# Optimization experiments

Measured on AMD Instinct MI355X. Metric: run time of the kernel, lower is better.

The kernel has to match this reference:

```python
import jax, jax.numpy as jnp
import numpy as np

DIM = 512          # model dim
DH = 32            # dim_head
WSZ = 8            # window_size
HEADS = DIM // DH  # 16
INNER = HEADS * DH # 512
D4 = DIM // 4      # DPB hidden = 128
EPS = 1e-5


def _ln(x, g, b=None, eps=EPS):
    m = jnp.mean(x, axis=-1, keepdims=True)
    v = jnp.var(x, axis=-1, keepdims=True)
    y = (x - m) * jax.lax.rsqrt(v + eps) * g
    return y if b is None else y + b


def setup_inputs() -> dict:
    key = jax.random.key(0)
    ks = jax.random.split(key, 8)
    g = lambda k, shape, s=0.02: (jax.random.normal(k, shape, jnp.float32) * s)
    return {
        "x": jax.random.normal(ks[0], (16, 64, 64, DIM), jnp.float32),
        "norm_g": jnp.ones((DIM,), jnp.float32),
        "norm_b": jnp.zeros((DIM,), jnp.float32),
        "w_qkv": g(ks[1], (DIM, 3 * INNER)),
        "w_out": g(ks[2], (INNER, DIM)),
        "b_out": jnp.zeros((DIM,), jnp.float32),
        "dpb_w0": g(ks[3], (2, D4)), "dpb_b0": jnp.zeros((D4,), jnp.float32), "dpb_ln0": jnp.ones((D4,), jnp.float32),
        "dpb_w1": g(ks[4], (D4, D4)), "dpb_b1": jnp.zeros((D4,), jnp.float32), "dpb_ln1": jnp.ones((D4,), jnp.float32),
        "dpb_w2": g(ks[5], (D4, D4)), "dpb_b2": jnp.zeros((D4,), jnp.float32), "dpb_ln2": jnp.ones((D4,), jnp.float32),
        "dpb_w3": g(ks[6], (D4, 1)), "dpb_b3": jnp.zeros((1,), jnp.float32),
    }


def reference(x, norm_g, norm_b, w_qkv, w_out, b_out,
              dpb_w0, dpb_b0, dpb_ln0,
              dpb_w1, dpb_b1, dpb_ln1,
              dpb_w2, dpb_b2, dpb_ln2,
              dpb_w3, dpb_b3):
    B, H, W, d = x.shape
    w = WSZ
    scale = DH ** -0.5

    x = _ln(x, norm_g, norm_b)

    # 'short' attention: partition into non-overlapping wxw windows
    # b (h s1) (w s2) d -> (b h w) s1 s2 d
    xw = x.reshape(B, H // w, w, W // w, w, d).transpose(0, 1, 3, 2, 4, 5)
    xw = xw.reshape(-1, w, w, d)  # [nb, w, w, d]

    qkv = xw @ w_qkv  # 1x1 conv == dense, no bias
    q, k, v = jnp.split(qkv, 3, axis=-1)
    to_heads = lambda t: t.reshape(t.shape[0], w * w, HEADS, DH).transpose(0, 2, 1, 3)
    q, k, v = map(to_heads, (q, k, v))  # [nb, h, w*w, dh]

    sim = jnp.einsum('bhid,bhjd->bhij', q * scale, k)  # [nb, h, w*w, w*w]

    # relative-position gather indices (static)
    pos = jnp.arange(w)
    grid = jnp.stack(jnp.meshgrid(pos, pos, indexing='ij'), axis=-1).reshape(-1, 2)
    rel = grid[:, None] - grid[None, :] + (w - 1)
    rel_pos_indices = rel[..., 0] * (2 * w - 1) + rel[..., 1]  # [w*w, w*w]

    # dynamic position bias MLP over the (2w+1)^2 relative offsets
    p = jnp.arange(-w, w + 1)
    rp = jnp.stack(jnp.meshgrid(p, p, indexing='ij'), axis=-1).reshape(-1, 2).astype(jnp.float32)
    h = jax.nn.relu(_ln(rp @ dpb_w0 + dpb_b0, dpb_ln0))
    h = jax.nn.relu(_ln(h @ dpb_w1 + dpb_b1, dpb_ln1))
    h = jax.nn.relu(_ln(h @ dpb_w2 + dpb_b2, dpb_ln2))
    biases = (h @ dpb_w3 + dpb_b3)[:, 0]  # [(2w+1)^2]

    sim = sim + biases[rel_pos_indices]
    attn = jax.nn.softmax(sim, axis=-1)
    out = jnp.einsum('bhij,bhjd->bhid', attn, v)

    out = out.transpose(0, 2, 1, 3).reshape(-1, w, w, INNER)
    out = out @ w_out + b_out  # 1x1 conv with bias

    # (b h w) s1 s2 d -> b (h s1) (w s2) d
    out = out.reshape(B, H // w, W // w, w, w, d).transpose(0, 1, 3, 2, 4, 5)
    return out.reshape(B, H, W, d)
```

## Files before the change

### kernel.cpp

```cpp
#include <hip/hip_runtime.h>
#include <cstdint>
#include <cstddef>

typedef unsigned short u16;
typedef __attribute__((ext_vector_type(8))) short short8;
typedef __attribute__((ext_vector_type(4))) float f32x4;
typedef __attribute__((ext_vector_type(4))) unsigned short us4;

#define AS1 __attribute__((address_space(1)))
#define AS3 __attribute__((address_space(3)))

__device__ __forceinline__ u16 f2bf(float f) {
  union { float f; unsigned u; } v; v.f = f;
  unsigned r = v.u + 0x7fffu + ((v.u >> 16) & 1u);
  return (u16)(r >> 16);
}

__device__ __forceinline__ void gload_lds16(const u16* g, u16* l) {
  __builtin_amdgcn_global_load_lds((AS1 void*)g, (AS3 void*)l, 16, 0, 0);
}

__global__ void ln_cast_kernel(const float* __restrict__ x, const float* __restrict__ g,
                               const float* __restrict__ b, u16* __restrict__ out) {
  const int lane = threadIdx.x & 63;
  const int tok = blockIdx.x * 4 + (threadIdx.x >> 6);
  const float4* row = (const float4*)(x + (size_t)tok * 512);
  float4 v0 = row[lane];
  float4 v1 = row[lane + 64];
  float s = v0.x + v0.y + v0.z + v0.w + v1.x + v1.y + v1.z + v1.w;
  float q = v0.x*v0.x + v0.y*v0.y + v0.z*v0.z + v0.w*v0.w
          + v1.x*v1.x + v1.y*v1.y + v1.z*v1.z + v1.w*v1.w;
#pragma unroll
  for (int m = 1; m < 64; m <<= 1) { s += __shfl_xor(s, m, 64); q += __shfl_xor(q, m, 64); }
  const float mean = s * (1.0f / 512.0f);
  const float var = q * (1.0f / 512.0f) - mean * mean;
  const float r = rsqrtf(var + 1e-5f);
  const float4* g4 = (const float4*)g;
  const float4* b4 = (const float4*)b;
  float4 ga = g4[lane], gb = g4[lane + 64];
  float4 ba = b4[lane], bb = b4[lane + 64];
  us4 o0 = { f2bf((v0.x - mean) * r * ga.x + ba.x), f2bf((v0.y - mean) * r * ga.y + ba.y),
             f2bf((v0.z - mean) * r * ga.z + ba.z), f2bf((v0.w - mean) * r * ga.w + ba.w) };
  us4 o1 = { f2bf((v1.x - mean) * r * gb.x + bb.x), f2bf((v1.y - mean) * r * gb.y + bb.y),
             f2bf((v1.z - mean) * r * gb.z + bb.z), f2bf((v1.w - mean) * r * gb.w + bb.w) };
  *(us4*)(out + (size_t)tok * 512 + lane * 4) = o0;
  *(us4*)(out + (size_t)tok * 512 + 256 + lane * 4) = o1;
}

__global__ void prep_w_kernel(const float* __restrict__ wqkv, const float* __restrict__ wout,
                              u16* __restrict__ wqkvT, u16* __restrict__ woutT) {
  int idx = blockIdx.x * blockDim.x + threadIdx.x;
  if (idx < 512 * 1536) {
    int n = idx >> 9, k = idx & 511;
    wqkvT[idx] = f2bf(wqkv[k * 1536 + n]);
  } else {
    int j = idx - 512 * 1536;
    if (j < 512 * 512) {
      int n = j >> 9, k = j & 511;
      woutT[j] = f2bf(wout[k * 512 + n]);
    }
  }
}

__device__ __forceinline__ float lnrelu128(float a, float g, float* red, int tid) {
  float s = a, q = a * a;
#pragma unroll
  for (int m = 1; m < 64; m <<= 1) { s += __shfl_xor(s, m, 64); q += __shfl_xor(q, m, 64); }
  __syncthreads();
  if ((tid & 63) == 0) { red[tid >> 6] = s; red[2 + (tid >> 6)] = q; }
  __syncthreads();
  float S = red[0] + red[1], Q = red[2] + red[3];
  float mean = S * (1.f / 128.f);
  float var = Q * (1.f / 128.f) - mean * mean;
  float y = (a - mean) * rsqrtf(var + 1e-5f) * g;
  return fmaxf(y, 0.f);
}

__global__ void dpb_mlp_kernel(const float* __restrict__ w0, const float* __restrict__ b0, const float* __restrict__ g0,
                               const float* __restrict__ w1, const float* __restrict__ b1, const float* __restrict__ g1,
                               const float* __restrict__ w2, const float* __restrict__ b2, const float* __restrict__ g2,
                               const float* __restrict__ w3, const float* __restrict__ b3,
                               float* __restrict__ biases) {
  __shared__ float h[128];
  __shared__ float red[4];
  const int tid = threadIdx.x;
  const int row = blockIdx.x;
  const float p0 = (float)(row / 17) - 8.0f;
  const float p1 = (float)(row % 17) - 8.0f;
  float a = p0 * w0[tid] + p1 * w0[128 + tid] + b0[tid];
  a = lnrelu128(a, g0[tid], red, tid);
  h[tid] = a;
  __syncthreads();
  float acc = b1[tid];
  for (int i = 0; i < 128; ++i) acc += h[i] * w1[i * 128 + tid];
  acc = lnrelu128(acc, g1[tid], red, tid);
  h[tid] = acc;
  __syncthreads();
  float acc2 = b2[tid];
  for (int i = 0; i < 128; ++i) acc2 += h[i] * w2[i * 128 + tid];
  acc2 = lnrelu128(acc2, g2[tid], red, tid);
  float t = acc2 * w3[tid];
#pragma unroll
  for (int m = 1; m < 64; m <<= 1) t += __shfl_xor(t, m, 64);
  __syncthreads();
  if ((tid & 63) == 0) red[tid >> 6] = t;
  __syncthreads();
  if (tid == 0) biases[row] = red[0] + red[1] + b3[0];
}

__global__ void dpb_table_kernel(const float* __restrict__ biases, float* __restrict__ table) {
  int t = blockIdx.x * blockDim.x + threadIdx.x;
  if (t < 4096) {
    int i = t >> 6, j = t & 63;
    int r0 = (i >> 3) - (j >> 3) + 7;
    int r1 = (i & 7) - (j & 7) + 7;
    table[t] = biases[r0 * 15 + r1];
  }
}

template <int CT, bool F32OUT>
__global__ __launch_bounds__(256, 4) void gemm128_kernel(const u16* __restrict__ A, const u16* __restrict__ BT,
                                                         void* __restrict__ Cv, const float* __restrict__ bias) {
  __shared__ __align__(16) u16 As[128 * 32];
  __shared__ __align__(16) u16 Bs[128 * 32];
  const int tid = threadIdx.x;
  const int w = tid >> 6, l = tid & 63;
  const int wr = w >> 1, wc = w & 1;
  const int cr = l & 15, cg = l >> 4;
  const int pc8 = (cg ^ ((cr + (cr >> 2)) & 3)) * 8;

  const int hw = blockIdx.x;
  const int ix = hw >> 3;
  const int rt = (hw & 7) + 8 * (ix / CT);
  const int ct = ix % CT;
  const size_t brow = (size_t)rt * 128;
  const size_t bcol = (size_t)ct * 128;
  const int N = CT * 128;

  const int srow = tid >> 2;
  const int csrc8 = ((tid & 3) ^ ((srow + (srow >> 2)) & 3)) * 8;
  const u16* gA = A + (brow + srow) * 512 + csrc8;
  const u16* gB = BT + (bcol + srow) * 512 + csrc8;

  const f32x4 zero = {0.f, 0.f, 0.f, 0.f};
  f32x4 acc[4][4];
#pragma unroll
  for (int i = 0; i < 4; ++i)
#pragma unroll
    for (int j = 0; j < 4; ++j) acc[i][j] = zero;

  const u16* aP = &As[(wr * 64 + cr) * 32 + pc8];
  const u16* bP = &Bs[(wc * 64 + cr) * 32 + pc8];

  for (int k0 = 0; k0 < 512; k0 += 32) {
    gload_lds16(gA + k0, &As[w * 512]);
    gload_lds16(gA + k0 + 64 * 512, &As[2048 + w * 512]);
    gload_lds16(gB + k0, &Bs[w * 512]);
    gload_lds16(gB + k0 + 64 * 512, &Bs[2048 + w * 512]);
    __syncthreads();
    short8 af[4], bf[4];
#pragma unroll
    for (int fr = 0; fr < 4; ++fr) af[fr] = *(const short8*)(aP + fr * 512);
#pragma unroll
    for (int fc = 0; fc < 4; ++fc) bf[fc] = *(const short8*)(bP + fc * 512);
#pragma unroll
    for (int fr = 0; fr < 4; ++fr)
#pragma unroll
      for (int fc = 0; fc < 4; ++fc)
        acc[fr][fc] = __builtin_amdgcn_mfma_f32_16x16x32_bf16(bf[fc], af[fr], acc[fr][fc], 0, 0, 0);
    __syncthreads();
  }

  if (F32OUT) {
    float* C = (float*)Cv;
#pragma unroll
    for (int fc = 0; fc < 4; ++fc) {
      size_t col = bcol + wc * 64 + fc * 16 + cg * 4;
      float4 bv = *(const float4*)&bias[col];
#pragma unroll
      for (int fr = 0; fr < 4; ++fr) {
        size_t r = brow + wr * 64 + fr * 16 + cr;
        float4 o = { acc[fr][fc][0] + bv.x, acc[fr][fc][1] + bv.y,
                     acc[fr][fc][2] + bv.z, acc[fr][fc][3] + bv.w };
        *(float4*)(C + r * N + col) = o;
      }
    }
  } else {
    u16* C = (u16*)Cv;
#pragma unroll
    for (int fc = 0; fc < 4; ++fc) {
      size_t col = bcol + wc * 64 + fc * 16 + cg * 4;
#pragma unroll
      for (int fr = 0; fr < 4; ++fr) {
        size_t r = brow + wr * 64 + fr * 16 + cr;
        uint2 p;
        p.x = (unsigned)f2bf(acc[fr][fc][0]) | ((unsigned)f2bf(acc[fr][fc][1]) << 16);
        p.y = (unsigned)f2bf(acc[fr][fc][2]) | ((unsigned)f2bf(acc[fr][fc][3]) << 16);
        *(uint2*)(C + r * N + col) = p;
      }
    }
  }
}

__global__ __launch_bounds__(64) void attn_kernel(const u16* __restrict__ qkv,
                                                  const float* __restrict__ table,
                                                  u16* __restrict__ aout) {
  __shared__ __align__(16) u16 P[64 * 72];
  __shared__ __align__(16) u16 VT[32 * 72];
  const int l = threadIdx.x;
  const int cr = l & 15, cg = l >> 4;
  const int head = blockIdx.x & 15;
  const int win = blockIdx.x >> 4;
  const int base = ((win >> 6) << 12) + (((win >> 3) & 7) << 9) + ((win & 7) << 3);

  {
    const size_t row = base + ((l >> 3) << 6) + (l & 7);
    const u16* vp = qkv + row * 1536 + 1024 + head * 32;
    short8 v0 = *(const short8*)(vp);
    short8 v1 = *(const short8*)(vp + 8);
    short8 v2 = *(const short8*)(vp + 16);
    short8 v3 = *(const short8*)(vp + 24);
#pragma unroll
    for (int j = 0; j < 8; ++j) {
      VT[j * 72 + l] = (u16)v0[j];
      VT[(8 + j) * 72 + l] = (u16)v1[j];
      VT[(16 + j) * 72 + l] = (u16)v2[j];
      VT[(24 + j) * 72 + l] = (u16)v3[j];
    }
  }

  short8 qf[4], kf[4];
#pragma unroll
  for (int mt = 0; mt < 4; ++mt) {
    int t = mt * 16 + cr;
    size_t row = base + ((t >> 3) << 6) + (t & 7);
    qf[mt] = *(const short8*)(qkv + row * 1536 + head * 32 + cg * 8);
    kf[mt] = *(const short8*)(qkv + row * 1536 + 512 + head * 32 + cg * 8);
  }

  const f32x4 zero = {0.f, 0.f, 0.f, 0.f};
  f32x4 s[4][4];
#pragma unroll
  for (int mt = 0; mt < 4; ++mt)
#pragma unroll
    for (int nt = 0; nt < 4; ++nt)
      s[mt][nt] = __builtin_amdgcn_mfma_f32_16x16x32_bf16(qf[mt], kf[nt], zero, 0, 0, 0);

  const float scale = 0.17677669529663689f;
#pragma unroll
  for (int mt = 0; mt < 4; ++mt) {
#pragma unroll
    for (int reg = 0; reg < 4; ++reg) {
      const int r = mt * 16 + cg * 4 + reg;
      float v[4];
      float mx = -3.0e38f;
#pragma unroll
      for (int nt = 0; nt < 4; ++nt) {
        v[nt] = s[mt][nt][reg] * scale + table[r * 64 + nt * 16 + cr];
        mx = fmaxf(mx, v[nt]);
      }
#pragma unroll
      for (int m2 = 1; m2 < 16; m2 <<= 1) mx = fmaxf(mx, __shfl_xor(mx, m2, 64));
      float sum = 0.f;
#pragma unroll
      for (int nt = 0; nt < 4; ++nt) { v[nt] = __expf(v[nt] - mx); sum += v[nt]; }
#pragma unroll
      for (int m2 = 1; m2 < 16; m2 <<= 1) sum += __shfl_xor(sum, m2, 64);
      float inv = 1.0f / sum;
#pragma unroll
      for (int nt = 0; nt < 4; ++nt) P[r * 72 + nt * 16 + cr] = f2bf(v[nt] * inv);
    }
  }
  __syncthreads();

  f32x4 o[4][2];
#pragma unroll
  for (int mt = 0; mt < 4; ++mt) { o[mt][0] = zero; o[mt][1] = zero; }
#pragma unroll
  for (int kk = 0; kk < 2; ++kk) {
    short8 pf[4], vf[2];
#pragma unroll
    for (int mt = 0; mt < 4; ++mt) pf[mt] = *(const short8*)&P[(mt * 16 + cr) * 72 + kk * 32 + cg * 8];
#pragma unroll
    for (int n2 = 0; n2 < 2; ++n2) vf[n2] = *(const short8*)&VT[(n2 * 16 + cr) * 72 + kk * 32 + cg * 8];
#pragma unroll
    for (int mt = 0; mt < 4; ++mt)
#pragma unroll
      for (int n2 = 0; n2 < 2; ++n2)
        o[mt][n2] = __builtin_amdgcn_mfma_f32_16x16x32_bf16(pf[mt], vf[n2], o[mt][n2], 0, 0, 0);
  }

#pragma unroll
  for (int mt = 0; mt < 4; ++mt)
#pragma unroll
    for (int n2 = 0; n2 < 2; ++n2)
#pragma unroll
      for (int reg = 0; reg < 4; ++reg) {
        int t = mt * 16 + cg * 4 + reg;
        size_t row = base + ((t >> 3) << 6) + (t & 7);
        aout[row * 512 + head * 32 + n2 * 16 + cr] = f2bf(o[mt][n2][reg]);
      }
}

extern "C" void kernel_launch(void* const* d_in, const int* in_sizes, int n_in,
                              void* d_out, int out_size, void* d_ws, size_t ws_size,
                              hipStream_t stream) {
  const float* x = (const float*)d_in[0];
  const float* norm_g = (const float*)d_in[1];
  const float* norm_b = (const float*)d_in[2];
  const float* w_qkv = (const float*)d_in[3];
  const float* w_out = (const float*)d_in[4];
  const float* b_out = (const float*)d_in[5];
  const float* dw0 = (const float*)d_in[6];
  const float* db0 = (const float*)d_in[7];
  const float* dg0 = (const float*)d_in[8];
  const float* dw1 = (const float*)d_in[9];
  const float* db1 = (const float*)d_in[10];
  const float* dg1 = (const float*)d_in[11];
  const float* dw2 = (const float*)d_in[12];
  const float* db2 = (const float*)d_in[13];
  const float* dg2 = (const float*)d_in[14];
  const float* dw3 = (const float*)d_in[15];
  const float* db3 = (const float*)d_in[16];

  char* ws = (char*)d_ws;
  size_t off = 0;
  auto take = [&](size_t bytes) { char* p = ws + off; off += (bytes + 255) & ~(size_t)255; return p; };
  u16* xln = (u16*)take(65536ull * 512 * 2);
  u16* wqkvT = (u16*)take(1536 * 512 * 2);
  u16* woutT = (u16*)take(512 * 512 * 2);
  float* biases = (float*)take(289 * 4);
  float* table = (float*)take(4096 * 4);

  size_t rem = (ws_size > off) ? ws_size - off : 0;
  int nch = 4;
  if (rem >= 65536ull * 2048 * 2 + 512) nch = 1;
  else if (rem >= 32768ull * 2048 * 2 + 512) nch = 2;
  const int rows = 65536 / nch;
  u16* qkvbuf = (u16*)take((size_t)rows * 1536 * 2);
  u16* attnbuf = (u16*)take((size_t)rows * 512 * 2);

  ln_cast_kernel<<<16384, 256, 0, stream>>>(x, norm_g, norm_b, xln);
  prep_w_kernel<<<4096, 256, 0, stream>>>(w_qkv, w_out, wqkvT, woutT);
  dpb_mlp_kernel<<<289, 128, 0, stream>>>(dw0, db0, dg0, dw1, db1, dg1, dw2, db2, dg2, dw3, db3, biases);
  dpb_table_kernel<<<16, 256, 0, stream>>>(biases, table);

  for (int c = 0; c < nch; ++c) {
    const u16* Ac = xln + (size_t)c * rows * 512;
    gemm128_kernel<12, false><<<(rows / 128) * 12, 256, 0, stream>>>(Ac, wqkvT, (void*)qkvbuf, nullptr);
    attn_kernel<<<(rows / 64) * 16, 64, 0, stream>>>(qkvbuf, table, attnbuf);
    float* Cc = (float*)d_out + (size_t)c * rows * 512;
    gemm128_kernel<4, true><<<(rows / 128) * 4, 256, 0, stream>>>(attnbuf, woutT, (void*)Cc, b_out);
  }
}
```

Before: 384.4 us.

## Load GEMM fragments directly from global memory with register double buffering

Replaces the LDS-staged GEMM (global_load_lds plus barriers) with each wave loading its MFMA operand fragments straight from global memory into registers, double-buffered two K-steps ahead. This removes the LDS traffic and the __syncthreads barriers. The cost is redundant global/L2 reads, because waves sharing rows no longer share a tile, and more register use; launch_bounds occupancy drops from 4 to 3 blocks. The grouped block-index swizzle for L2 locality is also replaced by a plain row-major tile order.

```diff
diff --git a/kernel.cpp b/kernel.cpp
--- a/kernel.cpp
+++ b/kernel.cpp
@@ -7,17 +7,10 @@
 typedef __attribute__((ext_vector_type(4))) float f32x4;
 typedef __attribute__((ext_vector_type(4))) unsigned short us4;
 
-#define AS1 __attribute__((address_space(1)))
-#define AS3 __attribute__((address_space(3)))
-
 __device__ __forceinline__ u16 f2bf(float f) {
   union { float f; unsigned u; } v; v.f = f;
   unsigned r = v.u + 0x7fffu + ((v.u >> 16) & 1u);
   return (u16)(r >> 16);
-}
-
-__device__ __forceinline__ void gload_lds16(const u16* g, u16* l) {
-  __builtin_amdgcn_global_load_lds((AS1 void*)g, (AS3 void*)l, 16, 0, 0);
 }
 
 __global__ void ln_cast_kernel(const float* __restrict__ x, const float* __restrict__ g,
@@ -119,28 +112,21 @@
 }
 
 template <int CT, bool F32OUT>
-__global__ __launch_bounds__(256, 4) void gemm128_kernel(const u16* __restrict__ A, const u16* __restrict__ BT,
-                                                         void* __restrict__ Cv, const float* __restrict__ bias) {
-  __shared__ __align__(16) u16 As[128 * 32];
-  __shared__ __align__(16) u16 Bs[128 * 32];
+__global__ __launch_bounds__(256, 3) void gemm_direct_kernel(const u16* __restrict__ A, const u16* __restrict__ BT,
+                                                             void* __restrict__ Cv, const float* __restrict__ bias) {
   const int tid = threadIdx.x;
   const int w = tid >> 6, l = tid & 63;
   const int wr = w >> 1, wc = w & 1;
   const int cr = l & 15, cg = l >> 4;
-  const int pc8 = (cg ^ ((cr + (cr >> 2)) & 3)) * 8;
 
   const int hw = blockIdx.x;
-  const int ix = hw >> 3;
-  const int rt = (hw & 7) + 8 * (ix / CT);
-  const int ct = ix % CT;
+  const int rt = hw / CT, ct = hw % CT;
   const size_t brow = (size_t)rt * 128;
   const size_t bcol = (size_t)ct * 128;
   const int N = CT * 128;
 
-  const int srow = tid >> 2;
-  const int csrc8 = ((tid & 3) ^ ((srow + (srow >> 2)) & 3)) * 8;
-  const u16* gA = A + (brow + srow) * 512 + csrc8;
-  const u16* gB = BT + (bcol + srow) * 512 + csrc8;
+  const u16* aB = A + (brow + wr * 64 + cr) * 512 + cg * 8;
+  const u16* bB = BT + (bcol + wc * 64 + cr) * 512 + cg * 8;
 
   const f32x4 zero = {0.f, 0.f, 0.f, 0.f};
   f32x4 acc[4][4];
@@ -149,27 +135,30 @@
 #pragma unroll
     for (int j = 0; j < 4; ++j) acc[i][j] = zero;
 
-  const u16* aP = &As[(wr * 64 + cr) * 32 + pc8];
-  const u16* bP = &Bs[(wc * 64 + cr) * 32 + pc8];
-
-  for (int k0 = 0; k0 < 512; k0 += 32) {
-    gload_lds16(gA + k0, &As[w * 512]);
-    gload_lds16(gA + k0 + 64 * 512, &As[2048 + w * 512]);
-    gload_lds16(gB + k0, &Bs[w * 512]);
-    gload_lds16(gB + k0 + 64 * 512, &Bs[2048 + w * 512]);
-    __syncthreads();
-    short8 af[4], bf[4];
-#pragma unroll
-    for (int fr = 0; fr < 4; ++fr) af[fr] = *(const short8*)(aP + fr * 512);
-#pragma unroll
-    for (int fc = 0; fc < 4; ++fc) bf[fc] = *(const short8*)(bP + fc * 512);
+  short8 af[2][4], bf[2][4];
+
+#define LOADK(BUF, K0)                                                              \
+  do {                                                                              \
+    _Pragma("unroll") for (int fr = 0; fr < 4; ++fr)                                \
+        af[BUF][fr] = *(const short8*)(aB + fr * 16 * 512 + (K0));                  \
+    _Pragma("unroll") for (int fc = 0; fc < 4; ++fc)                                \
+        bf[BUF][fc] = *(const short8*)(bB + fc * 16 * 512 + (K0));                  \
+  } while (0)
+
+  LOADK(0, 0);
+  LOADK(1, 32);
+
+#pragma unroll
+  for (int kk = 0; kk < 16; ++kk) {
+    const int cur = kk & 1;
 #pragma unroll
     for (int fr = 0; fr < 4; ++fr)
 #pragma unroll
       for (int fc = 0; fc < 4; ++fc)
-        acc[fr][fc] = __builtin_amdgcn_mfma_f32_16x16x32_bf16(bf[fc], af[fr], acc[fr][fc], 0, 0, 0);
-    __syncthreads();
-  }
+        acc[fr][fc] = __builtin_amdgcn_mfma_f32_16x16x32_bf16(bf[cur][fc], af[cur][fr], acc[fr][fc], 0, 0, 0);
+    if (kk < 14) LOADK(cur, (kk + 2) * 32);
+  }
+#undef LOADK
 
   if (F32OUT) {
     float* C = (float*)Cv;
@@ -347,9 +336,9 @@
 
   for (int c = 0; c < nch; ++c) {
     const u16* Ac = xln + (size_t)c * rows * 512;
-    gemm128_kernel<12, false><<<(rows / 128) * 12, 256, 0, stream>>>(Ac, wqkvT, (void*)qkvbuf, nullptr);
+    gemm_direct_kernel<12, false><<<(rows / 128) * 12, 256, 0, stream>>>(Ac, wqkvT, (void*)qkvbuf, nullptr);
     attn_kernel<<<(rows / 64) * 16, 64, 0, stream>>>(qkvbuf, table, attnbuf);
     float* Cc = (float*)d_out + (size_t)c * rows * 512;
-    gemm128_kernel<4, true><<<(rows / 128) * 4, 256, 0, stream>>>(attnbuf, woutT, (void*)Cc, b_out);
-  }
-}
+    gemm_direct_kernel<4, true><<<(rows / 128) * 4, 256, 0, stream>>>(attnbuf, woutT, (void*)Cc, b_out);
+  }
+}
```

Result: slower. 678.3 us (+76.5%).

## Keep attention probabilities in registers via transposed S and lane shuffles

Applied to the files above, without the earlier changes.

The attention kernel now computes S transposed (K·Q^T) so each lane holds a key column. The softmax reduces across fewer lanes and the probabilities are rearranged into MFMA operands with cross-lane shuffles, instead of being staged through LDS behind a barrier. Four window-head pairs now share one 256-thread block, each with its own V^T slice. The bias table is read with float4 loads and the output is written as packed 4-element stores. This removes LDS round-trips and the block sync, at the cost of more shuffle instructions and higher register pressure.

```diff
diff --git a/kernel.cpp b/kernel.cpp
--- a/kernel.cpp
+++ b/kernel.cpp
@@ -202,16 +202,18 @@
   }
 }
 
-__global__ __launch_bounds__(64) void attn_kernel(const u16* __restrict__ qkv,
-                                                  const float* __restrict__ table,
-                                                  u16* __restrict__ aout) {
-  __shared__ __align__(16) u16 P[64 * 72];
-  __shared__ __align__(16) u16 VT[32 * 72];
-  const int l = threadIdx.x;
+__global__ __launch_bounds__(256, 3) void attn_kernel(const u16* __restrict__ qkv,
+                                                      const float* __restrict__ table,
+                                                      u16* __restrict__ aout) {
+  __shared__ __align__(16) u16 VT[4][32 * 72];
+  const int l = threadIdx.x & 63;
+  const int wv = threadIdx.x >> 6;
+  const int pair = blockIdx.x * 4 + wv;
+  const int head = pair & 15;
+  const int win = pair >> 4;
+  const int base = ((win >> 6) << 12) + (((win >> 3) & 7) << 9) + ((win & 7) << 3);
   const int cr = l & 15, cg = l >> 4;
-  const int head = blockIdx.x & 15;
-  const int win = blockIdx.x >> 4;
-  const int base = ((win >> 6) << 12) + (((win >> 3) & 7) << 9) + ((win & 7) << 3);
+  u16* vt = VT[wv];
 
   {
     const size_t row = base + ((l >> 3) << 6) + (l & 7);
@@ -222,20 +224,20 @@
     short8 v3 = *(const short8*)(vp + 24);
 #pragma unroll
     for (int j = 0; j < 8; ++j) {
-      VT[j * 72 + l] = (u16)v0[j];
-      VT[(8 + j) * 72 + l] = (u16)v1[j];
-      VT[(16 + j) * 72 + l] = (u16)v2[j];
-      VT[(24 + j) * 72 + l] = (u16)v3[j];
+      vt[j * 72 + l] = (u16)v0[j];
+      vt[(8 + j) * 72 + l] = (u16)v1[j];
+      vt[(16 + j) * 72 + l] = (u16)v2[j];
+      vt[(24 + j) * 72 + l] = (u16)v3[j];
     }
   }
 
   short8 qf[4], kf[4];
 #pragma unroll
-  for (int mt = 0; mt < 4; ++mt) {
-    int t = mt * 16 + cr;
+  for (int i = 0; i < 4; ++i) {
+    int t = i * 16 + cr;
     size_t row = base + ((t >> 3) << 6) + (t & 7);
-    qf[mt] = *(const short8*)(qkv + row * 1536 + head * 32 + cg * 8);
-    kf[mt] = *(const short8*)(qkv + row * 1536 + 512 + head * 32 + cg * 8);
+    qf[i] = *(const short8*)(qkv + row * 1536 + head * 32 + cg * 8);
+    kf[i] = *(const short8*)(qkv + row * 1536 + 512 + head * 32 + cg * 8);
   }
 
   const f32x4 zero = {0.f, 0.f, 0.f, 0.f};
@@ -244,62 +246,86 @@
   for (int mt = 0; mt < 4; ++mt)
 #pragma unroll
     for (int nt = 0; nt < 4; ++nt)
-      s[mt][nt] = __builtin_amdgcn_mfma_f32_16x16x32_bf16(qf[mt], kf[nt], zero, 0, 0, 0);
+      s[mt][nt] = __builtin_amdgcn_mfma_f32_16x16x32_bf16(kf[mt], qf[nt], zero, 0, 0, 0);
+
+  asm volatile("s_waitcnt lgkmcnt(0)" ::: "memory");
+  __builtin_amdgcn_sched_barrier(0);
+  short8 vfT[2][2];
+#pragma unroll
+  for (int dt = 0; dt < 2; ++dt)
+#pragma unroll
+    for (int kk = 0; kk < 2; ++kk)
+      vfT[dt][kk] = *(const short8*)&vt[(dt * 16 + cr) * 72 + kk * 32 + cg * 8];
 
   const float scale = 0.17677669529663689f;
-#pragma unroll
-  for (int mt = 0; mt < 4; ++mt) {
-#pragma unroll
-    for (int reg = 0; reg < 4; ++reg) {
-      const int r = mt * 16 + cg * 4 + reg;
-      float v[4];
-      float mx = -3.0e38f;
-#pragma unroll
-      for (int nt = 0; nt < 4; ++nt) {
-        v[nt] = s[mt][nt][reg] * scale + table[r * 64 + nt * 16 + cr];
-        mx = fmaxf(mx, v[nt]);
+  f32x4 o[2][4];
+#pragma unroll
+  for (int dt = 0; dt < 2; ++dt)
+#pragma unroll
+    for (int nt = 0; nt < 4; ++nt) o[dt][nt] = zero;
+
+  const int laneA = cr + 32 * (cg & 1);
+  const int hi = cg >> 1;
+
+#pragma unroll
+  for (int nt = 0; nt < 4; ++nt) {
+    float p[16];
+    float mx = -3.0e38f;
+#pragma unroll
+    for (int mt = 0; mt < 4; ++mt) {
+      float4 tb = *(const float4*)&table[(nt * 16 + cr) * 64 + mt * 16 + cg * 4];
+      p[mt * 4 + 0] = s[mt][nt][0] * scale + tb.x;
+      p[mt * 4 + 1] = s[mt][nt][1] * scale + tb.y;
+      p[mt * 4 + 2] = s[mt][nt][2] * scale + tb.z;
+      p[mt * 4 + 3] = s[mt][nt][3] * scale + tb.w;
+      mx = fmaxf(mx, fmaxf(fmaxf(p[mt * 4], p[mt * 4 + 1]), fmaxf(p[mt * 4 + 2], p[mt * 4 + 3])));
+    }
+    mx = fmaxf(mx, __shfl_xor(mx, 16, 64));
+    mx = fmaxf(mx, __shfl_xor(mx, 32, 64));
+    float sum = 0.f;
+#pragma unroll
+    for (int i = 0; i < 16; ++i) { p[i] = __expf(p[i] - mx); sum += p[i]; }
+    sum += __shfl_xor(sum, 16, 64);
+    sum += __shfl_xor(sum, 32, 64);
+    const float inv = 1.0f / sum;
+
+    unsigned pk[4][2];
+#pragma unroll
+    for (int mt = 0; mt < 4; ++mt)
+#pragma unroll
+      for (int i = 0; i < 2; ++i)
+        pk[mt][i] = (unsigned)f2bf(p[mt * 4 + 2 * i] * inv) | ((unsigned)f2bf(p[mt * 4 + 2 * i + 1] * inv) << 16);
+
+#pragma unroll
+    for (int kk = 0; kk < 2; ++kk) {
+      union { unsigned u[4]; short8 v; } pf;
+#pragma unroll
+      for (int i = 0; i < 2; ++i) {
+        unsigned x0 = (unsigned)__shfl((int)pk[2 * kk][i], laneA, 64);
+        unsigned x1 = (unsigned)__shfl((int)pk[2 * kk + 1][i], laneA, 64);
+        unsigned y0 = (unsigned)__shfl((int)pk[2 * kk][i], laneA + 16, 64);
+        unsigned y1 = (unsigned)__shfl((int)pk[2 * kk + 1][i], laneA + 16, 64);
+        pf.u[i] = hi ? x1 : x0;
+        pf.u[2 + i] = hi ? y1 : y0;
       }
 #pragma unroll
-      for (int m2 = 1; m2 < 16; m2 <<= 1) mx = fmaxf(mx, __shfl_xor(mx, m2, 64));
-      float sum = 0.f;
-#pragma unroll
-      for (int nt = 0; nt < 4; ++nt) { v[nt] = __expf(v[nt] - mx); sum += v[nt]; }
-#pragma unroll
-      for (int m2 = 1; m2 < 16; m2 <<= 1) sum += __shfl_xor(sum, m2, 64);
-      float inv = 1.0f / sum;
-#pragma unroll
-      for (int nt = 0; nt < 4; ++nt) P[r * 72 + nt * 16 + cr] = f2bf(v[nt] * inv);
-    }
-  }
-  __syncthreads();
-
-  f32x4 o[4][2];
-#pragma unroll
-  for (int mt = 0; mt < 4; ++mt) { o[mt][0] = zero; o[mt][1] = zero; }
-#pragma unroll
-  for (int kk = 0; kk < 2; ++kk) {
-    short8 pf[4], vf[2];
-#pragma unroll
-    for (int mt = 0; mt < 4; ++mt) pf[mt] = *(const short8*)&P[(mt * 16 + cr) * 72 + kk * 32 + cg * 8];
-#pragma unroll
-    for (int n2 = 0; n2 < 2; ++n2) vf[n2] = *(const short8*)&VT[(n2 * 16 + cr) * 72 + kk * 32 + cg * 8];
-#pragma unroll
-    for (int mt = 0; mt < 4; ++mt)
-#pragma unroll
-      for (int n2 = 0; n2 < 2; ++n2)
-        o[mt][n2] = __builtin_amdgcn_mfma_f32_16x16x32_bf16(pf[mt], vf[n2], o[mt][n2], 0, 0, 0);
-  }
-
-#pragma unroll
-  for (int mt = 0; mt < 4; ++mt)
-#pragma unroll
-    for (int n2 = 0; n2 < 2; ++n2)
-#pragma unroll
-      for (int reg = 0; reg < 4; ++reg) {
-        int t = mt * 16 + cg * 4 + reg;
-        size_t row = base + ((t >> 3) << 6) + (t & 7);
-        aout[row * 512 + head * 32 + n2 * 16 + cr] = f2bf(o[mt][n2][reg]);
-      }
+      for (int dt = 0; dt < 2; ++dt)
+        o[dt][nt] = __builtin_amdgcn_mfma_f32_16x16x32_bf16(vfT[dt][kk], pf.v, o[dt][nt], 0, 0, 0);
+    }
+  }
+
+#pragma unroll
+  for (int nt = 0; nt < 4; ++nt) {
+    int t = nt * 16 + cr;
+    size_t row = base + ((t >> 3) << 6) + (t & 7);
+#pragma unroll
+    for (int dt = 0; dt < 2; ++dt) {
+      uint2 pck;
+      pck.x = (unsigned)f2bf(o[dt][nt][0]) | ((unsigned)f2bf(o[dt][nt][1]) << 16);
+      pck.y = (unsigned)f2bf(o[dt][nt][2]) | ((unsigned)f2bf(o[dt][nt][3]) << 16);
+      *(uint2*)(aout + row * 512 + head * 32 + dt * 16 + cg * 4) = pck;
+    }
+  }
 }
 
 extern "C" void kernel_launch(void* const* d_in, const int* in_sizes, int n_in,
@@ -348,7 +374,7 @@
   for (int c = 0; c < nch; ++c) {
     const u16* Ac = xln + (size_t)c * rows * 512;
     gemm128_kernel<12, false><<<(rows / 128) * 12, 256, 0, stream>>>(Ac, wqkvT, (void*)qkvbuf, nullptr);
-    attn_kernel<<<(rows / 64) * 16, 64, 0, stream>>>(qkvbuf, table, attnbuf);
+    attn_kernel<<<(rows / 64) * 16 / 4, 256, 0, stream>>>(qkvbuf, table, attnbuf);
     float* Cc = (float*)d_out + (size_t)c * rows * 512;
     gemm128_kernel<4, true><<<(rows / 128) * 4, 256, 0, stream>>>(attnbuf, woutT, (void*)Cc, b_out);
   }
```

After: 366.2 us. -4.7%, faster.
